# Optimization experiments

Hardware: AMD Instinct MI355X
Metric: run time of the kernel (lower is better)

The kernel has to match this reference:

```python
import jax, jax.numpy as jnp
import numpy as np

B, C, N = 16, 256, 2048
D = C // 8  # q/k channel dim = 32
EPS = 1e-5
NEG_SLOPE = 0.2


def _conv1x1(x, w, b):
    # x: [B,C,N], w: [O,C], b: [O] -> [B,O,N]
    return jnp.einsum('oc,bcn->bon', w, x) + b[None, :, None]


def _bn(y, gamma, beta):
    # BatchNorm1d training-mode: per-channel stats over (batch, length)
    m = y.mean(axis=(0, 2), keepdims=True)
    v = y.var(axis=(0, 2), keepdims=True)  # biased, matches torch normalization
    return (y - m) * jax.lax.rsqrt(v + EPS) * gamma[None, :, None] + beta[None, :, None]


def setup_inputs() -> dict:
    key = jax.random.key(0)
    ks = jax.random.split(key, 14)
    s_qk = 1.0 / np.sqrt(C)
    return {
        'x': jax.random.normal(ks[0], (B, C, N), dtype=jnp.float32),
        'q_w': jax.random.normal(ks[1], (D, C), dtype=jnp.float32) * s_qk,
        'q_b': jnp.zeros((D,), jnp.float32),
        'q_g': jnp.ones((D,), jnp.float32),
        'q_be': jnp.zeros((D,), jnp.float32),
        'k_w': jax.random.normal(ks[2], (D, C), dtype=jnp.float32) * s_qk,
        'k_b': jnp.zeros((D,), jnp.float32),
        'k_g': jnp.ones((D,), jnp.float32),
        'k_be': jnp.zeros((D,), jnp.float32),
        'v_w': jax.random.normal(ks[3], (C, C), dtype=jnp.float32) * s_qk,
        'v_b': jnp.zeros((C,), jnp.float32),
        'v_g': jnp.ones((C,), jnp.float32),
        'v_be': jnp.zeros((C,), jnp.float32),
    }


def reference(x, q_w, q_b, q_g, q_be, k_w, k_b, k_g, k_be, v_w, v_b, v_g, v_be):
    # q, k: conv1x1 -> BN (no activation); v: conv1x1 -> BN -> LeakyReLU(0.2)
    q = _bn(_conv1x1(x, q_w, q_b), q_g, q_be)          # [B,D,N]
    k = _bn(_conv1x1(x, k_w, k_b), k_g, k_be)          # [B,D,N]
    v = jax.nn.leaky_relu(_bn(_conv1x1(x, v_w, v_b), v_g, v_be), NEG_SLOPE)  # [B,C,N]
    energy = jnp.einsum('bdn,bdm->bnm', q, k)          # [B,N,N]
    attn = jax.nn.softmax(energy, axis=-1)
    o = jnp.einsum('bcm,bnm->bcn', v, attn)            # attn applied over points
    return o + x
```

## Files before the change

kernel.cpp:

```cpp
#include <hip/hip_runtime.h>

#define BATCH 16
#define CH    256
#define NPT   2048
#define DQK   32
#define OTOT  320
#define EPSB  1e-5f
#define SLOPE 0.2f

typedef __attribute__((ext_vector_type(8))) short bf16x8;
typedef __attribute__((ext_vector_type(4))) float f32x4;

__device__ __forceinline__ unsigned short f2bf(float f) {
    unsigned u = __float_as_uint(f);
    u = (u + 0x7FFFu + ((u >> 16) & 1u)) >> 16;
    return (unsigned short)u;
}
__device__ __forceinline__ float bf2f(unsigned short h) {
    return __uint_as_float(((unsigned)h) << 16);
}
__device__ __forceinline__ unsigned cvt_pk_bf16(float a, float b) {
    unsigned r;
    asm("v_cvt_pk_bf16_f32 %0, %1, %2" : "=v"(r) : "v"(a), "v"(b));
    return r;
}

__global__ __launch_bounds__(256) void prep_kernel(
    const float* __restrict__ qw, const float* __restrict__ qb,
    const float* __restrict__ kw, const float* __restrict__ kb,
    const float* __restrict__ vw, const float* __restrict__ vb,
    unsigned short* __restrict__ Whi, unsigned short* __restrict__ Wlo,
    float* __restrict__ Bv)
{
    int idx = blockIdx.x * 256 + threadIdx.x;
    int o = idx >> 8, c = idx & 255;
    float w;
    if (o < 32)      w = qw[(size_t)o * CH + c];
    else if (o < 64) w = kw[(size_t)(o - 32) * CH + c];
    else             w = vw[(size_t)(o - 64) * CH + c];
    unsigned short wh = f2bf(w);
    float rem = w - bf2f(wh);
    Whi[idx] = wh;
    Wlo[idx] = f2bf(rem);
    if (idx < OTOT) {
        int oo = idx;
        float bb;
        if (oo < 32)      bb = qb[oo];
        else if (oo < 64) bb = kb[oo - 32];
        else              bb = vb[oo - 64];
        Bv[oo] = bb;
    }
}

__global__ __launch_bounds__(256) void conv_kernel(
    const float* __restrict__ x,
    const unsigned short* __restrict__ Whi, const unsigned short* __restrict__ Wlo,
    const float* __restrict__ Bv,
    unsigned short* __restrict__ Ybf,
    float* __restrict__ Sum, float* __restrict__ Sq)
{
    int lin = blockIdx.x;
    int vid = (lin & 7) * 160 + (lin >> 3);
    int o5  = vid % 5;
    int rem = vid / 5;
    int ob = o5 * 64;
    int n0 = (rem & 15) * 128;
    int b  = rem >> 4;

    int tid = threadIdx.x;
    int w = tid >> 6, lane = tid & 63;
    int quad = lane >> 4, l16 = lane & 15;
    int wo = w >> 1, wn = w & 1;

    __shared__ unsigned short Xh[128][40];
    __shared__ unsigned short Xl[128][40];

    int nl = tid & 127;
    int ch = tid >> 7;
    const float* xb = x + (size_t)b * CH * NPT + n0 + nl;

    f32x4 acc[2][4];
#pragma unroll
    for (int ot = 0; ot < 2; ++ot)
#pragma unroll
        for (int nt = 0; nt < 4; ++nt)
            acc[ot][nt] = (f32x4){0.f, 0.f, 0.f, 0.f};

    float xv[16];
#pragma unroll
    for (int i = 0; i < 16; ++i)
        xv[i] = xb[(size_t)(ch * 16 + i) * NPT];

    for (int ks = 0; ks < 8; ++ks) {
        __syncthreads();
#pragma unroll
        for (int g = 0; g < 4; ++g) {
            ushort4 h4, l4;
            unsigned short* ph = (unsigned short*)&h4;
            unsigned short* pl = (unsigned short*)&l4;
#pragma unroll
            for (int j = 0; j < 4; ++j) {
                float f = xv[g * 4 + j];
                unsigned short h = f2bf(f);
                ph[j] = h;
                pl[j] = f2bf(f - bf2f(h));
            }
            *(ushort4*)&Xh[nl][ch * 16 + g * 4] = h4;
            *(ushort4*)&Xl[nl][ch * 16 + g * 4] = l4;
        }
        __syncthreads();

        if (ks < 7) {
#pragma unroll
            for (int i = 0; i < 16; ++i)
                xv[i] = xb[(size_t)((ks + 1) * 32 + ch * 16 + i) * NPT];
        }

        bf16x8 ah[2], al[2];
#pragma unroll
        for (int ot = 0; ot < 2; ++ot) {
            size_t orow = (size_t)(ob + wo * 32 + ot * 16 + l16) * 256 + ks * 32 + quad * 8;
            ah[ot] = *(const bf16x8*)(Whi + orow);
            al[ot] = *(const bf16x8*)(Wlo + orow);
        }
#pragma unroll
        for (int nt = 0; nt < 4; ++nt) {
            int nr = wn * 64 + nt * 16 + l16;
            bf16x8 bh = *(const bf16x8*)&Xh[nr][quad * 8];
            bf16x8 bl = *(const bf16x8*)&Xl[nr][quad * 8];
#pragma unroll
            for (int ot = 0; ot < 2; ++ot) {
                acc[ot][nt] = __builtin_amdgcn_mfma_f32_16x16x32_bf16(ah[ot], bh, acc[ot][nt], 0, 0, 0);
                acc[ot][nt] = __builtin_amdgcn_mfma_f32_16x16x32_bf16(ah[ot], bl, acc[ot][nt], 0, 0, 0);
                acc[ot][nt] = __builtin_amdgcn_mfma_f32_16x16x32_bf16(al[ot], bh, acc[ot][nt], 0, 0, 0);
            }
        }
    }

#pragma unroll
    for (int ot = 0; ot < 2; ++ot) {
        int obase = ob + wo * 32 + ot * 16 + quad * 4;
        float bias[4], sv[4], sq[4];
#pragma unroll
        for (int r = 0; r < 4; ++r) {
            bias[r] = Bv[obase + r];
            sv[r] = 0.f; sq[r] = 0.f;
        }
#pragma unroll
        for (int nt = 0; nt < 4; ++nt) {
            int n = n0 + wn * 64 + nt * 16 + l16;
#pragma unroll
            for (int r = 0; r < 4; ++r) {
                float v = acc[ot][nt][r] + bias[r];
                Ybf[((size_t)b * OTOT + obase + r) * NPT + n] = f2bf(v);
                sv[r] += v; sq[r] += v * v;
            }
        }
#pragma unroll
        for (int r = 0; r < 4; ++r) {
            float a = sv[r], q = sq[r];
            a += __shfl_xor(a, 1); q += __shfl_xor(q, 1);
            a += __shfl_xor(a, 2); q += __shfl_xor(q, 2);
            a += __shfl_xor(a, 4); q += __shfl_xor(q, 4);
            a += __shfl_xor(a, 8); q += __shfl_xor(q, 8);
            if (l16 == 0) {
                atomicAdd(&Sum[obase + r], a);
                atomicAdd(&Sq[obase + r], q);
            }
        }
    }
}

__global__ __launch_bounds__(256) void pack_kernel(
    const unsigned short* __restrict__ Ybf,
    const float* __restrict__ Sum, const float* __restrict__ Sq,
    const float* __restrict__ qg, const float* __restrict__ qbe,
    const float* __restrict__ kg, const float* __restrict__ kbe,
    const float* __restrict__ vg, const float* __restrict__ vbe,
    unsigned short* __restrict__ QKt, unsigned short* __restrict__ Vbf)
{
    int b = blockIdx.y, n0 = blockIdx.x * 64;
    int tid = threadIdx.x;

    __shared__ float sA[OTOT], sC[OTOT];
    for (int o = tid; o < OTOT; o += 256) {
        const float inv = 1.0f / (BATCH * NPT);
        float mean = Sum[o] * inv;
        float var  = Sq[o] * inv - mean * mean;
        float g, be;
        if (o < 32)      { g = qg[o];      be = qbe[o];      }
        else if (o < 64) { g = kg[o - 32]; be = kbe[o - 32]; }
        else             { g = vg[o - 64]; be = vbe[o - 64]; }
        float a = g * rsqrtf(var + EPSB);
        sA[o] = a;
        sC[o] = be - mean * a;
    }
    __syncthreads();

    for (int e = tid; e < 4096; e += 256) {
        int c = e >> 4, n4 = (e & 15) * 4;
        ushort4 v4 = *(const ushort4*)(Ybf + ((size_t)b * OTOT + 64 + c) * NPT + n0 + n4);
        float a = sA[64 + c], cc = sC[64 + c];
        ushort4 w4;
        unsigned short* pi = (unsigned short*)&v4;
        unsigned short* po = (unsigned short*)&w4;
#pragma unroll
        for (int i = 0; i < 4; ++i) {
            float y = bf2f(pi[i]) * a + cc;
            y = (y > 0.f) ? y : SLOPE * y;
            po[i] = f2bf(y);
        }
        *(ushort4*)(Vbf + ((size_t)b * CH + c) * NPT + n0 + n4) = w4;
    }

    __shared__ unsigned short T[64][72];
    for (int e = tid; e < 1024; e += 256) {
        int o = e >> 4, n4 = (e & 15) * 4;
        ushort4 v4 = *(const ushort4*)(Ybf + ((size_t)b * OTOT + o) * NPT + n0 + n4);
        float a = sA[o], cc = sC[o];
        unsigned short* pi = (unsigned short*)&v4;
#pragma unroll
        for (int i = 0; i < 4; ++i)
            T[n4 + i][o] = f2bf(bf2f(pi[i]) * a + cc);
    }
    __syncthreads();
    for (int e = tid; e < 1024; e += 256) {
        int nn = e >> 4, o4 = (e & 15) * 4;
        ushort4 v4 = *(const ushort4*)&T[nn][o4];
        *(ushort4*)(QKt + ((size_t)b * NPT + n0 + nn) * 64 + o4) = v4;
    }
}

__global__ __launch_bounds__(256, 4) void attn_kernel(
    const unsigned short* __restrict__ QKt,
    const unsigned short* __restrict__ Vbf,
    const float* __restrict__ x,
    float* __restrict__ out)
{
    int L = blockIdx.x;
    int xcd = L & 7, k = L >> 3;
    int gi = k >> 5, n0i = k & 31;
    int grp = xcd * 4 + gi;
    int b = grp >> 1, z = grp & 1;
    int n0 = n0i * 64;

    int tid = threadIdx.x;
    int w = tid >> 6, lane = tid & 63;
    int quad = lane >> 4, l16 = lane & 15;

    const unsigned short* QK = QKt + (size_t)b * NPT * 64;
    const unsigned short* V  = Vbf + ((size_t)b * CH + z * 128) * NPT;

    __shared__ unsigned short Pbf[2][64][72];
    __shared__ float rsw[4][64];
    __shared__ float rtot[64];

    bf16x8 qa[4];
#pragma unroll
    for (int nt = 0; nt < 4; ++nt)
        qa[nt] = *(const bf16x8*)(QK + ((size_t)(n0 + nt * 16 + l16)) * 64 + quad * 8);

    f32x4 acc[4][2];
#pragma unroll
    for (int nt = 0; nt < 4; ++nt)
#pragma unroll
        for (int ct = 0; ct < 2; ++ct)
            acc[nt][ct] = (f32x4){0.f, 0.f, 0.f, 0.f};

    float rsum[4];
#pragma unroll
    for (int nt = 0; nt < 4; ++nt) rsum[nt] = 0.f;

    const f32x4 zero4 = (f32x4){0.f, 0.f, 0.f, 0.f};

    bf16x8 kb = *(const bf16x8*)(QK + ((size_t)(w * 16 + l16)) * 64 + 32 + quad * 8);

    for (int mt = 0; mt < NPT / 64; ++mt) {
        unsigned short (*Pb)[72] = Pbf[mt & 1];

        f32x4 s[4];
#pragma unroll
        for (int nt = 0; nt < 4; ++nt)
            s[nt] = __builtin_amdgcn_mfma_f32_16x16x32_bf16(kb, qa[nt], zero4, 0, 0, 0);

        if (mt < NPT / 64 - 1)
            kb = *(const bf16x8*)(QK + ((size_t)((mt + 1) * 64 + w * 16 + l16)) * 64 + 32 + quad * 8);

#pragma unroll
        for (int nt = 0; nt < 4; ++nt) {
            float p0 = __expf(s[nt][0]);
            float p1 = __expf(s[nt][1]);
            float p2 = __expf(s[nt][2]);
            float p3 = __expf(s[nt][3]);
            rsum[nt] += (p0 + p1) + (p2 + p3);
            uint2 dd;
            dd.x = cvt_pk_bf16(p0, p1);
            dd.y = cvt_pk_bf16(p2, p3);
            *(uint2*)&Pb[nt * 16 + l16][w * 16 + quad * 4] = dd;
        }

        __syncthreads();

#pragma unroll
        for (int ks = 0; ks < 2; ++ks) {
            bf16x8 pa[4];
#pragma unroll
            for (int nt = 0; nt < 4; ++nt)
                pa[nt] = *(const bf16x8*)&Pb[nt * 16 + l16][ks * 32 + quad * 8];
#pragma unroll
            for (int ct = 0; ct < 2; ++ct) {
                const unsigned short* vp =
                    V + ((size_t)(w * 32 + ct * 16 + l16)) * NPT + mt * 64 + ks * 32 + quad * 8;
                bf16x8 vb = *(const bf16x8*)vp;
#pragma unroll
                for (int nt = 0; nt < 4; ++nt)
                    acc[nt][ct] = __builtin_amdgcn_mfma_f32_16x16x32_bf16(pa[nt], vb, acc[nt][ct], 0, 0, 0);
            }
        }
    }

#pragma unroll
    for (int nt = 0; nt < 4; ++nt) {
        float v = rsum[nt];
        v += __shfl_xor(v, 16);
        v += __shfl_xor(v, 32);
        if (lane < 16) rsw[w][nt * 16 + lane] = v;
    }
    __syncthreads();
    if (tid < 64)
        rtot[tid] = 1.0f / (rsw[0][tid] + rsw[1][tid] + rsw[2][tid] + rsw[3][tid]);
    __syncthreads();

    float rin[4][4];
#pragma unroll
    for (int nt = 0; nt < 4; ++nt)
#pragma unroll
        for (int r = 0; r < 4; ++r) rin[nt][r] = rtot[nt * 16 + quad * 4 + r];

#pragma unroll
    for (int nt = 0; nt < 4; ++nt)
#pragma unroll
        for (int ct = 0; ct < 2; ++ct) {
            int c = z * 128 + w * 32 + ct * 16 + l16;
            int n = n0 + nt * 16 + quad * 4;
            size_t gi4 = ((size_t)b * CH + c) * NPT + n;
            float4 xv = *(const float4*)(x + gi4);
            float4 o;
            o.x = acc[nt][ct][0] * rin[nt][0] + xv.x;
            o.y = acc[nt][ct][1] * rin[nt][1] + xv.y;
            o.z = acc[nt][ct][2] * rin[nt][2] + xv.z;
            o.w = acc[nt][ct][3] * rin[nt][3] + xv.w;
            *(float4*)(out + gi4) = o;
        }
}

extern "C" void kernel_launch(void* const* d_in, const int* in_sizes, int n_in,
                              void* d_out, int out_size, void* d_ws, size_t ws_size,
                              hipStream_t stream)
{
    const float* x   = (const float*)d_in[0];
    const float* qw  = (const float*)d_in[1];
    const float* qb  = (const float*)d_in[2];
    const float* qg  = (const float*)d_in[3];
    const float* qbe = (const float*)d_in[4];
    const float* kw  = (const float*)d_in[5];
    const float* kb  = (const float*)d_in[6];
    const float* kg  = (const float*)d_in[7];
    const float* kbe = (const float*)d_in[8];
    const float* vw  = (const float*)d_in[9];
    const float* vb  = (const float*)d_in[10];
    const float* vg  = (const float*)d_in[11];
    const float* vbe = (const float*)d_in[12];
    float* out = (float*)d_out;

    unsigned short* Ybf = (unsigned short*)d_ws;
    unsigned short* QKt = Ybf + (size_t)BATCH * OTOT * NPT;
    unsigned short* Vbf = QKt + (size_t)BATCH * NPT * 64;
    float* tail = (float*)(Vbf + (size_t)BATCH * CH * NPT);
    float* Sum = tail;
    float* Sq  = tail + OTOT;
    unsigned short* Whi = QKt;
    unsigned short* Wlo = Whi + (size_t)CH * OTOT;
    float* Bv = (float*)(Wlo + (size_t)CH * OTOT);

    hipMemsetAsync(Sum, 0, 2 * OTOT * sizeof(float), stream);
    prep_kernel <<<320, 256, 0, stream>>>(qw, qb, kw, kb, vw, vb, Whi, Wlo, Bv);
    conv_kernel <<<1280, 256, 0, stream>>>(x, Whi, Wlo, Bv, Ybf, Sum, Sq);
    pack_kernel <<<dim3(NPT / 64, BATCH), 256, 0, stream>>>(
        Ybf, Sum, Sq, qg, qbe, kg, kbe, vg, vbe, QKt, Vbf);
    attn_kernel <<<1024, 256, 0, stream>>>(QKt, Vbf, x, out);
}
```

Baseline: 270.9 us.

## Keep softmax probabilities in registers and split PV reduction across waves

The attention kernel no longer writes exp(scores) to shared memory and synchronises each tile. Each wave now feeds its own 16-key slice of probabilities straight from registers into 16x16x16 bf16 MFMAs against all 128 value channels. Partial outputs are then reduced across the four waves through shared memory at the end. This removes the per-tile LDS round-trip and barrier, but quadruples the accumulator registers (occupancy hint lowered to 2), uses smaller MFMAs, does narrower V loads, and adds a serialized four-phase epilogue reduction.

```diff
diff --git a/kernel.cpp b/kernel.cpp
--- a/kernel.cpp
+++ b/kernel.cpp
@@ -9,6 +9,7 @@
 #define SLOPE 0.2f
 
 typedef __attribute__((ext_vector_type(8))) short bf16x8;
+typedef __attribute__((ext_vector_type(4))) short bf16x4;
 typedef __attribute__((ext_vector_type(4))) float f32x4;
 
 __device__ __forceinline__ unsigned short f2bf(float f) {
@@ -23,6 +24,10 @@
     unsigned r;
     asm("v_cvt_pk_bf16_f32 %0, %1, %2" : "=v"(r) : "v"(a), "v"(b));
     return r;
+}
+__device__ __forceinline__ void mfma16_bf16(f32x4& acc, bf16x4 a, bf16x4 b) {
+    asm volatile("v_mfma_f32_16x16x16_bf16 %0, %1, %2, %0"
+                 : "+v"(acc) : "v"(a), "v"(b));
 }
 
 __global__ __launch_bounds__(256) void prep_kernel(
@@ -231,7 +236,7 @@
     }
 }
 
-__global__ __launch_bounds__(256, 4) void attn_kernel(
+__global__ __launch_bounds__(256, 2) void attn_kernel(
     const unsigned short* __restrict__ QKt,
     const unsigned short* __restrict__ Vbf,
     const float* __restrict__ x,
@@ -251,7 +256,7 @@
     const unsigned short* QK = QKt + (size_t)b * NPT * 64;
     const unsigned short* V  = Vbf + ((size_t)b * CH + z * 128) * NPT;
 
-    __shared__ unsigned short Pbf[2][64][72];
+    __shared__ float Red[3][64][33];
     __shared__ float rsw[4][64];
     __shared__ float rtot[64];
 
@@ -260,11 +265,11 @@
     for (int nt = 0; nt < 4; ++nt)
         qa[nt] = *(const bf16x8*)(QK + ((size_t)(n0 + nt * 16 + l16)) * 64 + quad * 8);
 
-    f32x4 acc[4][2];
+    f32x4 acc[4][8];
 #pragma unroll
     for (int nt = 0; nt < 4; ++nt)
 #pragma unroll
-        for (int ct = 0; ct < 2; ++ct)
+        for (int ct = 0; ct < 8; ++ct)
             acc[nt][ct] = (f32x4){0.f, 0.f, 0.f, 0.f};
 
     float rsum[4];
@@ -275,9 +280,9 @@
 
     bf16x8 kb = *(const bf16x8*)(QK + ((size_t)(w * 16 + l16)) * 64 + 32 + quad * 8);
 
+    const unsigned short* Vl = V + (size_t)l16 * NPT + w * 16 + quad * 4;
+
     for (int mt = 0; mt < NPT / 64; ++mt) {
-        unsigned short (*Pb)[72] = Pbf[mt & 1];
-
         f32x4 s[4];
 #pragma unroll
         for (int nt = 0; nt < 4; ++nt)
@@ -286,6 +291,7 @@
         if (mt < NPT / 64 - 1)
             kb = *(const bf16x8*)(QK + ((size_t)((mt + 1) * 64 + w * 16 + l16)) * 64 + 32 + quad * 8);
 
+        bf16x4 pa[4];
 #pragma unroll
         for (int nt = 0; nt < 4; ++nt) {
             float p0 = __expf(s[nt][0]);
@@ -293,29 +299,19 @@
             float p2 = __expf(s[nt][2]);
             float p3 = __expf(s[nt][3]);
             rsum[nt] += (p0 + p1) + (p2 + p3);
-            uint2 dd;
-            dd.x = cvt_pk_bf16(p0, p1);
-            dd.y = cvt_pk_bf16(p2, p3);
-            *(uint2*)&Pb[nt * 16 + l16][w * 16 + quad * 4] = dd;
-        }
-
-        __syncthreads();
-
-#pragma unroll
-        for (int ks = 0; ks < 2; ++ks) {
-            bf16x8 pa[4];
-#pragma unroll
-            for (int nt = 0; nt < 4; ++nt)
-                pa[nt] = *(const bf16x8*)&Pb[nt * 16 + l16][ks * 32 + quad * 8];
-#pragma unroll
-            for (int ct = 0; ct < 2; ++ct) {
-                const unsigned short* vp =
-                    V + ((size_t)(w * 32 + ct * 16 + l16)) * NPT + mt * 64 + ks * 32 + quad * 8;
-                bf16x8 vb = *(const bf16x8*)vp;
-#pragma unroll
-                for (int nt = 0; nt < 4; ++nt)
-                    acc[nt][ct] = __builtin_amdgcn_mfma_f32_16x16x32_bf16(pa[nt], vb, acc[nt][ct], 0, 0, 0);
-            }
+            union { unsigned u[2]; bf16x4 v; } cv;
+            cv.u[0] = cvt_pk_bf16(p0, p1);
+            cv.u[1] = cvt_pk_bf16(p2, p3);
+            pa[nt] = cv.v;
+        }
+
+#pragma unroll
+        for (int ct = 0; ct < 8; ++ct) {
+            bf16x4 vb = *(const bf16x4*)(Vl + (size_t)(ct * 16) * NPT + mt * 64);
+            mfma16_bf16(acc[0][ct], pa[0], vb);
+            mfma16_bf16(acc[1][ct], pa[1], vb);
+            mfma16_bf16(acc[2][ct], pa[2], vb);
+            mfma16_bf16(acc[3][ct], pa[3], vb);
         }
     }
 
@@ -331,27 +327,45 @@
         rtot[tid] = 1.0f / (rsw[0][tid] + rsw[1][tid] + rsw[2][tid] + rsw[3][tid]);
     __syncthreads();
 
-    float rin[4][4];
-#pragma unroll
-    for (int nt = 0; nt < 4; ++nt)
-#pragma unroll
-        for (int r = 0; r < 4; ++r) rin[nt][r] = rtot[nt * 16 + quad * 4 + r];
-
-#pragma unroll
-    for (int nt = 0; nt < 4; ++nt)
-#pragma unroll
-        for (int ct = 0; ct < 2; ++ct) {
-            int c = z * 128 + w * 32 + ct * 16 + l16;
-            int n = n0 + nt * 16 + quad * 4;
-            size_t gi4 = ((size_t)b * CH + c) * NPT + n;
-            float4 xv = *(const float4*)(x + gi4);
-            float4 o;
-            o.x = acc[nt][ct][0] * rin[nt][0] + xv.x;
-            o.y = acc[nt][ct][1] * rin[nt][1] + xv.y;
-            o.z = acc[nt][ct][2] * rin[nt][2] + xv.z;
-            o.w = acc[nt][ct][3] * rin[nt][3] + xv.w;
-            *(float4*)(out + gi4) = o;
-        }
+#pragma unroll
+    for (int ph = 0; ph < 4; ++ph) {
+        if (w != ph) {
+            int slot = (w < ph) ? w : w - 1;
+#pragma unroll
+            for (int ct = 0; ct < 8; ++ct)
+#pragma unroll
+                for (int r = 0; r < 4; ++r)
+                    Red[slot][lane][ct * 4 + r] = acc[ph][ct][r];
+        }
+        __syncthreads();
+        if (w == ph) {
+#pragma unroll
+            for (int slot = 0; slot < 3; ++slot)
+#pragma unroll
+                for (int ct = 0; ct < 8; ++ct)
+#pragma unroll
+                    for (int r = 0; r < 4; ++r)
+                        acc[ph][ct][r] += Red[slot][lane][ct * 4 + r];
+            float rin[4];
+#pragma unroll
+            for (int r = 0; r < 4; ++r)
+                rin[r] = rtot[ph * 16 + quad * 4 + r];
+            int n = n0 + ph * 16 + quad * 4;
+#pragma unroll
+            for (int ct = 0; ct < 8; ++ct) {
+                int c = z * 128 + ct * 16 + l16;
+                size_t gi4 = ((size_t)b * CH + c) * NPT + n;
+                float4 xv = *(const float4*)(x + gi4);
+                float4 o;
+                o.x = acc[ph][ct][0] * rin[0] + xv.x;
+                o.y = acc[ph][ct][1] * rin[1] + xv.y;
+                o.z = acc[ph][ct][2] * rin[2] + xv.z;
+                o.w = acc[ph][ct][3] * rin[3] + xv.w;
+                *(float4*)(out + gi4) = o;
+            }
+        }
+        __syncthreads();
+    }
 }
 
 extern "C" void kernel_launch(void* const* d_in, const int* in_sizes, int n_in,
```

Measured after the change: 374.4 us. 1.38x slower.
